# Performance work log

Hardware: AMD Instinct MI355X
Metric: run time of the kernel (lower is better)

Reference implementation:

```python
import jax, jax.numpy as jnp
import numpy as np

OUT_IMG = 256
OUT_MSK = 64


def _src_coords(n_out, size):
    # F.interpolate bilinear align_corners=False source coordinates, clamped to edge
    sizef = size.astype(jnp.float32)
    t = (jnp.arange(n_out, dtype=jnp.float32) + 0.5) * (sizef / n_out) - 0.5
    t = jnp.clip(t, 0.0, sizef - 1.0)
    t0 = jnp.floor(t).astype(jnp.int32)
    t1 = jnp.minimum(t0 + 1, size - 1)
    return t0, t1, t - t0.astype(jnp.float32)


def _per_sample(x_img, x_msk, x_bg, pad, sel, color):
    # x_img [3,H,W] float, x_msk [H,W] bool, x_bg [3,Hb,Wb], pad [4] int (l,r,t,b)
    H, W = x_msk.shape
    ys = jnp.any(x_msk, axis=1)
    xs = jnp.any(x_msk, axis=0)
    iy = jnp.arange(H)
    ix = jnp.arange(W)
    miny = jnp.min(jnp.where(ys, iy, H))
    maxy = jnp.max(jnp.where(ys, iy, -1))
    minx = jnp.min(jnp.where(xs, ix, W))
    maxx = jnp.max(jnp.where(xs, ix, -1))
    h = maxy - miny + 1
    w = maxx - minx + 1
    left, right, top, bot = pad[0], pad[1], pad[2], pad[3]
    Hp = h + top + bot   # padded crop height
    Wp = w + left + right  # padded crop width
    # background: real bg image or solid random color (c[ii][-1] > 2 branch)
    bg_sel = jnp.where(sel > 2, x_bg, jnp.broadcast_to(color[:, None, None], x_bg.shape))

    def mask_at(P, Q):
        # value of the padded-cropped mask at integer padded coords (P, Q)
        in_crop = (P >= top) & (P < top + h) & (Q >= left) & (Q < left + w)
        r = jnp.clip(miny + P - top, 0, H - 1)
        c = jnp.clip(minx + Q - left, 0, W - 1)
        return in_crop & x_msk[r, c], r, c

    def sample_img(py, px):
        # composited padded image at integer coords (py x px grid) -> [3,Ho,Wo]
        P = py[:, None]
        Q = px[None, :]
        m, r, c = mask_at(P, Q)
        iv = x_img[:, r, c]
        bv = bg_sel[:, P, Q]
        return jnp.where(m[None], iv, bv)

    def sample_msk(py, px):
        m, _, _ = mask_at(py[:, None], px[None, :])
        return m.astype(jnp.float32)

    def bilinear(sample_fn, n_out, ch_leading):
        y0, y1, wy = _src_coords(n_out, Hp)
        x0, x1, wx = _src_coords(n_out, Wp)
        s00 = sample_fn(y0, x0)
        s01 = sample_fn(y0, x1)
        s10 = sample_fn(y1, x0)
        s11 = sample_fn(y1, x1)
        wy_ = wy[:, None]
        wx_ = wx[None, :]
        if ch_leading:
            wy_ = wy_[None]
            wx_ = wx_[None]
        top_row = s00 * (1.0 - wx_) + s01 * wx_
        bot_row = s10 * (1.0 - wx_) + s11 * wx_
        return top_row * (1.0 - wy_) + bot_row * wy_

    img_out = bilinear(sample_img, OUT_IMG, True)        # [3,256,256]
    msk_out = bilinear(sample_msk, OUT_MSK, False)[None]  # [1,64,64]
    return img_out, msk_out


def _rgb_to_hsv(x):
    r, g, b = x[:, 0], x[:, 1], x[:, 2]
    mx = jnp.max(x, axis=1)
    mn = jnp.min(x, axis=1)
    d = mx - mn
    ds = jnp.where(d > 0, d, 1.0)
    hr = ((g - b) / ds) % 6.0
    hg = (b - r) / ds + 2.0
    hb = (r - g) / ds + 4.0
    hch = jnp.where(mx == r, hr, jnp.where(mx == g, hg, hb)) / 6.0
    hch = jnp.where(d > 0, hch, 0.0)
    s = jnp.where(mx > 0, d / jnp.where(mx > 0, mx, 1.0), 0.0)
    return hch, s, mx


def _hsv_to_rgb(hch, s, v):
    h6 = hch * 6.0
    i = jnp.floor(h6)
    f = h6 - i
    p = v * (1.0 - s)
    q = v * (1.0 - f * s)
    t = v * (1.0 - (1.0 - f) * s)
    im = i.astype(jnp.int32) % 6
    conds = [im == 0, im == 1, im == 2, im == 3, im == 4, im == 5]
    r = jnp.select(conds, [v, q, p, p, t, v])
    g = jnp.select(conds, [t, v, v, q, p, p])
    b = jnp.select(conds, [p, p, t, v, v, q])
    return jnp.stack([r, g, b], axis=1)


def _color_jitter(img, jit):
    # ColorJitter(0.1, 0.1, 0.1, 0.1) with explicit per-sample factors
    b = (0.9 + 0.2 * jit[:, 0])[:, None, None, None]
    c = (0.9 + 0.2 * jit[:, 1])[:, None, None, None]
    s = (0.9 + 0.2 * jit[:, 2])[:, None, None, None]
    hd = (-0.1 + 0.2 * jit[:, 3])[:, None, None]
    img = jnp.clip(img * b, 0.0, 1.0)
    gray = (0.299 * img[:, 0] + 0.587 * img[:, 1] + 0.114 * img[:, 2])[:, None]
    mean = jnp.mean(gray, axis=(2, 3), keepdims=True)
    img = jnp.clip(c * img + (1.0 - c) * mean, 0.0, 1.0)
    gray = (0.299 * img[:, 0] + 0.587 * img[:, 1] + 0.114 * img[:, 2])[:, None]
    img = jnp.clip(s * img + (1.0 - s) * gray, 0.0, 1.0)
    hch, sa, v = _rgb_to_hsv(img)
    hch = (hch + hd) % 1.0
    return jnp.clip(_hsv_to_rgb(hch, sa, v), 0.0, 1.0)


def setup_inputs() -> dict:
    key = jax.random.key(0)
    ks = jax.random.split(key, 7)
    B, H, W = 64, 448, 448
    return {
        "img": jax.random.uniform(ks[0], (B, 3, H, W), jnp.float32),
        "ms": jax.random.uniform(ks[1], (B, 1, H, W), jnp.float32),
        "bg": jax.random.uniform(ks[2], (B, 3, H + 40, W + 40), jnp.float32),
        "pads": jax.random.randint(ks[3], (B, 4), 0, 20, jnp.int32),
        "csel": jax.random.randint(ks[4], (B,), 0, 20, jnp.int32),
        "rand_color": jax.random.uniform(ks[5], (B, 3), jnp.float32),
        "jitter": jax.random.uniform(ks[6], (B, 4), jnp.float32),
    }


def reference(img, ms, bg, pads, csel, rand_color, jitter):
    mask = ms[:, 0] > 0.5
    img_out, msk_out = jax.vmap(_per_sample)(img, mask, bg, pads, csel, rand_color)
    img_out = _color_jitter(img_out, jitter)
    return img_out, msk_out
```

## Files before the change

kernel.cpp:

```cpp
#include <hip/hip_runtime.h>

#define H_IN 448
#define W_IN 448
#define HW_IN (H_IN * W_IN)
#define BGW 488
#define BGHW (BGW * BGW)
#define OUTI 256
#define OUTI_PIX (OUTI * OUTI)
#define OUTM 64
#define B_SAMPLES 64
#define BBOX_CHUNKS 16
#define BBOX_ROWS (H_IN / BBOX_CHUNKS)
#define BITS_STRIDE 8

typedef unsigned long long u64;

__device__ __forceinline__ float clamp01(float x) { return fminf(fmaxf(x, 0.f), 1.f); }
__device__ __forceinline__ int clampi(int x, int lo, int hi) { return min(max(x, lo), hi); }

__device__ __forceinline__ void gld_lds16(const float4* g, float4* l) {
    __builtin_amdgcn_global_load_lds(
        (const __attribute__((address_space(1))) void*)g,
        (__attribute__((address_space(3))) void*)l, 16, 0, 0);
}

__global__ void k_bbox(const float* __restrict__ ms, int* __restrict__ bbox,
                       u64* __restrict__ bits) {
    int b = blockIdx.y, chunk = blockIdx.x;
    int tid = threadIdx.x;
    int wave = tid >> 6, lane = tid & 63;
    const float* msB = ms + (size_t)b * HW_IN;
    u64* bitsB = bits + (size_t)b * H_IN * BITS_STRIDE;

    int miny = H_IN, maxy = -1, minx = W_IN, maxx = -1;
    for (int rr = wave; rr < BBOX_ROWS; rr += 4) {
        int row = chunk * BBOX_ROWS + rr;
        const float4* rowp = (const float4*)(msB + (size_t)row * W_IN);
#pragma unroll
        for (int sub = 0; sub < 2; ++sub) {
            int c4 = sub * 64 + lane;
            bool valid = c4 < (W_IN / 4);
            float4 v = rowp[min(c4, W_IN / 4 - 1)];
            bool a0 = valid && (v.x > 0.5f);
            bool a1 = valid && (v.y > 0.5f);
            bool a2 = valid && (v.z > 0.5f);
            bool a3 = valid && (v.w > 0.5f);
            u64 b0 = __ballot(a0), b1 = __ballot(a1), b2 = __ballot(a2), b3 = __ballot(a3);
            if (a0 | a1 | a2 | a3) {
                miny = min(miny, row); maxy = max(maxy, row);
                int xb = c4 * 4;
                if (a0) { minx = min(minx, xb);     maxx = max(maxx, xb); }
                if (a1) { minx = min(minx, xb + 1); maxx = max(maxx, xb + 1); }
                if (a2) { minx = min(minx, xb + 2); maxx = max(maxx, xb + 2); }
                if (a3) { minx = min(minx, xb + 3); maxx = max(maxx, xb + 3); }
            }
            if (lane < 4) {
                u64 w = (lane == 0) ? b0 : (lane == 1) ? b1 : (lane == 2) ? b2 : b3;
                bitsB[(size_t)row * BITS_STRIDE + sub * 4 + lane] = w;
            }
        }
    }
    __shared__ int s[4];
    if (tid == 0) { s[0] = H_IN; s[1] = -1; s[2] = W_IN; s[3] = -1; }
    __syncthreads();
    atomicMin(&s[0], miny); atomicMax(&s[1], maxy);
    atomicMin(&s[2], minx); atomicMax(&s[3], maxx);
    __syncthreads();
    if (tid == 0) {
        atomicMin(&bbox[b * 4 + 0], s[0]);
        atomicMin(&bbox[b * 4 + 1], -s[1]);
        atomicMin(&bbox[b * 4 + 2], s[2]);
        atomicMin(&bbox[b * 4 + 3], -s[3]);
    }
}

struct Geo {
    int miny, minx, h, w, top, left, Hp, Wp;
};
__device__ __forceinline__ Geo load_geo(const int* __restrict__ bbox,
                                        const int* __restrict__ pads, int b) {
    Geo g;
    g.miny = bbox[b * 4 + 0];
    int maxy = -bbox[b * 4 + 1];
    g.minx = bbox[b * 4 + 2];
    int maxx = -bbox[b * 4 + 3];
    int left = pads[b * 4 + 0], right = pads[b * 4 + 1];
    int top = pads[b * 4 + 2], bot = pads[b * 4 + 3];
    g.h = maxy - g.miny + 1;
    g.w = maxx - g.minx + 1;
    g.top = top; g.left = left;
    g.Hp = g.h + top + bot;
    g.Wp = g.w + left + right;
    return g;
}

__device__ __forceinline__ void src_coord(int i, int n_out, int size,
                                          int& t0, int& t1, float& frac) {
    float sizef = (float)size;
    float t = (i + 0.5f) * (sizef / (float)n_out) - 0.5f;
    t = fminf(fmaxf(t, 0.f), sizef - 1.f);
    t0 = (int)floorf(t);
    t1 = min(t0 + 1, size - 1);
    frac = t - (float)t0;
}

__device__ __forceinline__ bool mask_bit(const u64* rowbits, int c) {
    u64 w = rowbits[((c >> 8) << 2) | (c & 3)];
    return (w >> ((c >> 2) & 63)) & 1ULL;
}

__global__ void __launch_bounds__(256) k_resize_img(
        const float* __restrict__ img, const float* __restrict__ bg,
        const int* __restrict__ pads, const int* __restrict__ csel,
        const float* __restrict__ rcol, const float* __restrict__ jit,
        const int* __restrict__ bbox, const u64* __restrict__ bits,
        float* __restrict__ out, float* __restrict__ partials) {
    int oy = blockIdx.x;
    int b = blockIdx.y;
    int tid = threadIdx.x;
    int wave = tid >> 6, lane = tid & 63;

    Geo g = load_geo(bbox, pads, b);
    bool useBg = csel[b] > 2;
    float c0 = rcol[b * 3 + 0], c1 = rcol[b * 3 + 1], c2 = rcol[b * 3 + 2];
    float bfac = 0.9f + 0.2f * jit[b * 4 + 0];

    int y0, y1; float wy;
    src_coord(oy, OUTI, g.Hp, y0, y1, wy);
    int r0 = clampi(g.miny + y0 - g.top, 0, H_IN - 1);
    int r1 = clampi(g.miny + y1 - g.top, 0, H_IN - 1);
    bool incy0 = (y0 >= g.top) && (y0 < g.top + g.h);
    bool incy1 = (y1 >= g.top) && (y1 < g.top + g.h);

    __shared__ float s_im[6][W_IN];
    __shared__ float s_bg[6][BGW];
    __shared__ u64 s_bits[2][BITS_STRIDE];
    __shared__ float ls[4];

    const float* imB = img + (size_t)b * 3 * HW_IN;
    const u64* bitsB = bits + (size_t)b * H_IN * BITS_STRIDE;

#pragma unroll
    for (int k = 0; k < 3; ++k) {
        int item = wave + k * 4;
        int p = item >> 1;
        int ck = item & 1;
        int row = (p >= 3) ? r1 : r0;
        int ch = (p >= 3) ? (p - 3) : p;
        const float4* src =
            (const float4*)(imB + (size_t)ch * HW_IN + (size_t)row * W_IN) + ck * 64 + lane;
        float4* dst = (float4*)(&s_im[p][0]) + ck * 64;
        if (lane < (ck ? 48 : 64)) gld_lds16(src, dst);
    }
    if (useBg) {
        const float* bgB = bg + (size_t)b * 3 * BGHW;
#pragma unroll
        for (int k = 0; k < 3; ++k) {
            int item = wave + k * 4;
            int p = item >> 1;
            int ck = item & 1;
            int row = (p >= 3) ? y1 : y0;
            int ch = (p >= 3) ? (p - 3) : p;
            const float4* src =
                (const float4*)(bgB + (size_t)ch * BGHW + (size_t)row * BGW) + ck * 64 + lane;
            float4* dst = (float4*)(&s_bg[p][0]) + ck * 64;
            if (lane < (ck ? 58 : 64)) gld_lds16(src, dst);
        }
    }
    if (tid < 16) {
        int ky = tid >> 3, idx = tid & 7;
        s_bits[ky][idx] = bitsB[(size_t)(ky ? r1 : r0) * BITS_STRIDE + idx];
    }
    __syncthreads();

    int x0, x1; float wx;
    src_coord(tid, OUTI, g.Wp, x0, x1, wx);

    float acc0 = 0.f, acc1 = 0.f, acc2 = 0.f;
#pragma unroll
    for (int tap = 0; tap < 4; ++tap) {
        int ky = tap >> 1;
        int ky3 = ky * 3;
        int Q = (tap & 1) ? x1 : x0;
        float wgt = (ky ? wy : 1.f - wy) * ((tap & 1) ? wx : 1.f - wx);
        bool incy = ky ? incy1 : incy0;
        bool in_crop = incy && (Q >= g.left) && (Q < g.left + g.w);
        int c = clampi(g.minx + Q - g.left, 0, W_IN - 1);
        bool mm = in_crop && mask_bit(s_bits[ky], c);
        float i0 = s_im[ky3 + 0][c], i1 = s_im[ky3 + 1][c], i2 = s_im[ky3 + 2][c];
        float b0, b1, b2;
        if (useBg) {
            b0 = s_bg[ky3 + 0][Q]; b1 = s_bg[ky3 + 1][Q]; b2 = s_bg[ky3 + 2][Q];
        } else {
            b0 = c0; b1 = c1; b2 = c2;
        }
        acc0 += wgt * (mm ? i0 : b0);
        acc1 += wgt * (mm ? i1 : b1);
        acc2 += wgt * (mm ? i2 : b2);
    }
    float o0 = clamp01(acc0 * bfac);
    float o1 = clamp01(acc1 * bfac);
    float o2 = clamp01(acc2 * bfac);
    size_t o = (size_t)b * 3 * OUTI_PIX + (size_t)oy * OUTI + tid;
    out[o] = o0;
    out[o + OUTI_PIX] = o1;
    out[o + 2 * OUTI_PIX] = o2;

    float gsum = 0.299f * o0 + 0.587f * o1 + 0.114f * o2;
#pragma unroll
    for (int off = 32; off > 0; off >>= 1) gsum += __shfl_down(gsum, off, 64);
    int wid = tid >> 6, lane2 = tid & 63;
    if (lane2 == 0) ls[wid] = gsum;
    __syncthreads();
    if (tid == 0)
        partials[b * 256 + oy] = ls[0] + ls[1] + ls[2] + ls[3];
}

__global__ void k_resize_msk(const u64* __restrict__ bits, const int* __restrict__ pads,
                             const int* __restrict__ bbox, float* __restrict__ outm) {
    int b = blockIdx.y;
    int pix = blockIdx.x * blockDim.x + threadIdx.x;
    int oy = pix >> 6, ox = pix & 63;

    Geo g = load_geo(bbox, pads, b);
    int y0, y1, x0, x1; float wy, wx;
    src_coord(oy, OUTM, g.Hp, y0, y1, wy);
    src_coord(ox, OUTM, g.Wp, x0, x1, wx);

    const u64* bitsB = bits + (size_t)b * H_IN * BITS_STRIDE;
    float acc = 0.f;
#pragma unroll
    for (int tap = 0; tap < 4; ++tap) {
        int P = (tap & 2) ? y1 : y0;
        int Q = (tap & 1) ? x1 : x0;
        float wgt = ((tap & 2) ? wy : 1.f - wy) * ((tap & 1) ? wx : 1.f - wx);
        bool in_crop = (P >= g.top) && (P < g.top + g.h) && (Q >= g.left) && (Q < g.left + g.w);
        int r = clampi(g.miny + P - g.top, 0, H_IN - 1);
        int c = clampi(g.minx + Q - g.left, 0, W_IN - 1);
        bool mm = in_crop && mask_bit(bitsB + (size_t)r * BITS_STRIDE, c);
        acc += wgt * (mm ? 1.f : 0.f);
    }
    outm[(size_t)b * (OUTM * OUTM) + pix] = acc;
}

__device__ __forceinline__ void jitter_px(float& r, float& g, float& bl,
                                          float cc, float ssf, float hd, float mean) {
    r = clamp01(cc * r + (1.f - cc) * mean);
    g = clamp01(cc * g + (1.f - cc) * mean);
    bl = clamp01(cc * bl + (1.f - cc) * mean);
    float gray = 0.299f * r + 0.587f * g + 0.114f * bl;
    r = clamp01(ssf * r + (1.f - ssf) * gray);
    g = clamp01(ssf * g + (1.f - ssf) * gray);
    bl = clamp01(ssf * bl + (1.f - ssf) * gray);
    float mx = fmaxf(r, fmaxf(g, bl));
    float mn = fminf(r, fminf(g, bl));
    float d = mx - mn;
    float dsv = (d > 0.f) ? d : 1.f;
    float hch;
    if (mx == r) {
        float t = (g - bl) / dsv;
        t = fmodf(t, 6.f);
        if (t < 0.f) t += 6.f;
        hch = t;
    } else if (mx == g) {
        hch = (bl - r) / dsv + 2.f;
    } else {
        hch = (r - g) / dsv + 4.f;
    }
    hch = (d > 0.f) ? hch * (1.f / 6.f) : 0.f;
    float sat = (mx > 0.f) ? d / mx : 0.f;
    float v = mx;
    float hh = hch + hd;
    hh -= floorf(hh);
    float h6 = hh * 6.f;
    float fi = floorf(h6);
    float f = h6 - fi;
    float pp = v * (1.f - sat);
    float q = v * (1.f - f * sat);
    float t = v * (1.f - (1.f - f) * sat);
    int im = ((int)fi) % 6;
    float ro, go, bo;
    switch (im) {
        case 0: ro = v;  go = t;  bo = pp; break;
        case 1: ro = q;  go = v;  bo = pp; break;
        case 2: ro = pp; go = v;  bo = t;  break;
        case 3: ro = pp; go = q;  bo = v;  break;
        case 4: ro = t;  go = pp; bo = v;  break;
        default: ro = v; go = pp; bo = q;  break;
    }
    r = clamp01(ro); g = clamp01(go); bl = clamp01(bo);
}

__global__ void k_jitter(float* __restrict__ io, const float* __restrict__ jit,
                         const float* __restrict__ partials) {
    int b = blockIdx.y;
    int tid = threadIdx.x;

    float pv = partials[b * 256 + tid];
#pragma unroll
    for (int off = 32; off > 0; off >>= 1) pv += __shfl_down(pv, off, 64);
    __shared__ float ls[4];
    int wid = tid >> 6, lane = tid & 63;
    if (lane == 0) ls[wid] = pv;
    __syncthreads();
    float mean = (ls[0] + ls[1] + ls[2] + ls[3]) * (1.f / (float)OUTI_PIX);

    float cc = 0.9f + 0.2f * jit[b * 4 + 1];
    float ssf = 0.9f + 0.2f * jit[b * 4 + 2];
    float hd = -0.1f + 0.2f * jit[b * 4 + 3];

    int idx4 = blockIdx.x * blockDim.x + tid;
    float4* pr = (float4*)(io + (size_t)b * 3 * OUTI_PIX) + idx4;
    float4* pg = pr + OUTI_PIX / 4;
    float4* pb = pr + 2 * (OUTI_PIX / 4);
    float4 r = *pr, g = *pg, bl = *pb;

    jitter_px(r.x, g.x, bl.x, cc, ssf, hd, mean);
    jitter_px(r.y, g.y, bl.y, cc, ssf, hd, mean);
    jitter_px(r.z, g.z, bl.z, cc, ssf, hd, mean);
    jitter_px(r.w, g.w, bl.w, cc, ssf, hd, mean);

    *pr = r; *pg = g; *pb = bl;
}

extern "C" void kernel_launch(void* const* d_in, const int* in_sizes, int n_in,
                              void* d_out, int out_size, void* d_ws, size_t ws_size,
                              hipStream_t stream) {
    const float* img = (const float*)d_in[0];
    const float* ms = (const float*)d_in[1];
    const float* bg = (const float*)d_in[2];
    const int* pads = (const int*)d_in[3];
    const int* csel = (const int*)d_in[4];
    const float* rcol = (const float*)d_in[5];
    const float* jit = (const float*)d_in[6];
    float* out = (float*)d_out;

    int* bbox = (int*)d_ws;
    float* partials = (float*)((char*)d_ws + 1024);
    u64* bits = (u64*)((char*)d_ws + 1024 + B_SAMPLES * 256 * sizeof(float));
    float* outm = out + (size_t)B_SAMPLES * 3 * OUTI_PIX;

    hipMemsetAsync(bbox, 0x7F, B_SAMPLES * 4 * sizeof(int), stream);

    k_bbox<<<dim3(BBOX_CHUNKS, B_SAMPLES), 256, 0, stream>>>(ms, bbox, bits);
    k_resize_img<<<dim3(OUTI, B_SAMPLES), 256, 0, stream>>>(
        img, bg, pads, csel, rcol, jit, bbox, bits, out, partials);
    k_resize_msk<<<dim3((OUTM * OUTM) / 256, B_SAMPLES), 256, 0, stream>>>(
        bits, pads, bbox, outm);
    k_jitter<<<dim3(OUTI_PIX / 4 / 256, B_SAMPLES), 256, 0, stream>>>(out, jit, partials);
}
```

Baseline: 122.4 us.

## Process eight output rows per block with double-buffered async LDS staging

The image resize kernel now has each block handle eight consecutive output rows instead of one. It double-buffers the source image, background and mask-bit rows in LDS, prefetching the next row via global_load_lds while computing the current one, with hand-tuned vmcnt waits. The horizontal taps are also restructured to read adjacent LDS entries and lerp, and partial sums per block shrink to one per group. This trades launch and per-block setup overhead and load latency exposure for fewer blocks (less parallelism), doubled LDS use, and fragile manual waitcnt accounting.

```diff
diff --git a/kernel.cpp b/kernel.cpp
--- a/kernel.cpp
+++ b/kernel.cpp
@@ -12,8 +12,12 @@
 #define BBOX_CHUNKS 16
 #define BBOX_ROWS (H_IN / BBOX_CHUNKS)
 #define BITS_STRIDE 8
+#define RPB 8
+#define NGRP (OUTI / RPB)
 
 typedef unsigned long long u64;
+
+#define WAITV(N) asm volatile("s_waitcnt vmcnt(" #N ")" ::: "memory")
 
 __device__ __forceinline__ float clamp01(float x) { return fminf(fmaxf(x, 0.f), 1.f); }
 __device__ __forceinline__ int clampi(int x, int lo, int hi) { return min(max(x, lo), hi); }
@@ -104,9 +108,60 @@
     frac = t - (float)t0;
 }
 
-__device__ __forceinline__ bool mask_bit(const u64* rowbits, int c) {
+__device__ __forceinline__ bool bit_at(const u64* rowbits, int c) {
     u64 w = rowbits[((c >> 8) << 2) | (c & 3)];
     return (w >> ((c >> 2) & 63)) & 1ULL;
+}
+
+struct RowGeom {
+    int y0, y1, r0, r1;
+    float wy;
+    bool incy0, incy1;
+};
+__device__ __forceinline__ RowGeom row_geom(const Geo& g, int oy) {
+    RowGeom rg;
+    src_coord(oy, OUTI, g.Hp, rg.y0, rg.y1, rg.wy);
+    rg.r0 = clampi(g.miny + rg.y0 - g.top, 0, H_IN - 1);
+    rg.r1 = clampi(g.miny + rg.y1 - g.top, 0, H_IN - 1);
+    rg.incy0 = (rg.y0 >= g.top) && (rg.y0 < g.top + g.h);
+    rg.incy1 = (rg.y1 >= g.top) && (rg.y1 < g.top + g.h);
+    return rg;
+}
+
+__device__ __forceinline__ void stage_async(
+        const float* imB, const float* bgB, const u64* bitsB, bool useBg,
+        const RowGeom& rg, int wave, int lane,
+        float (*im)[W_IN], float (*bgp)[BGW], u64 (*bt)[BITS_STRIDE]) {
+#pragma unroll
+    for (int k = 0; k < 3; ++k) {
+        int chunk = wave * 3 + k;
+        int p = chunk >> 1, ck = chunk & 1;
+        int row = (p >= 3) ? rg.r1 : rg.r0;
+        int ch = (p >= 3) ? p - 3 : p;
+        const float4* src =
+            (const float4*)(imB + (size_t)ch * HW_IN + (size_t)row * W_IN) + ck * 64 + lane;
+        float4* dst = (float4*)(&im[p][0]) + ck * 64;
+        if (lane < (ck ? 48 : 64)) gld_lds16(src, dst);
+    }
+    if (useBg) {
+#pragma unroll
+        for (int k = 0; k < 3; ++k) {
+            int chunk = wave * 3 + k;
+            int p = chunk >> 1, ck = chunk & 1;
+            int row = (p >= 3) ? rg.y1 : rg.y0;
+            int ch = (p >= 3) ? p - 3 : p;
+            const float4* src =
+                (const float4*)(bgB + (size_t)ch * BGHW + (size_t)row * BGW) + ck * 64 + lane;
+            float4* dst = (float4*)(&bgp[p][0]) + ck * 64;
+            if (lane < (ck ? 58 : 64)) gld_lds16(src, dst);
+        }
+    }
+    if (wave < 2) {
+        int row = wave ? rg.r1 : rg.r0;
+        const float4* src = (const float4*)(bitsB + (size_t)row * BITS_STRIDE) + lane;
+        float4* dst = (float4*)(&bt[wave][0]);
+        if (lane < 4) gld_lds16(src, dst);
+    }
 }
 
 __global__ void __launch_bounds__(256) k_resize_img(
@@ -115,7 +170,7 @@
         const float* __restrict__ rcol, const float* __restrict__ jit,
         const int* __restrict__ bbox, const u64* __restrict__ bits,
         float* __restrict__ out, float* __restrict__ partials) {
-    int oy = blockIdx.x;
+    int grp = blockIdx.x;
     int b = blockIdx.y;
     int tid = threadIdx.x;
     int wave = tid >> 6, lane = tid & 63;
@@ -125,95 +180,94 @@
     float c0 = rcol[b * 3 + 0], c1 = rcol[b * 3 + 1], c2 = rcol[b * 3 + 2];
     float bfac = 0.9f + 0.2f * jit[b * 4 + 0];
 
-    int y0, y1; float wy;
-    src_coord(oy, OUTI, g.Hp, y0, y1, wy);
-    int r0 = clampi(g.miny + y0 - g.top, 0, H_IN - 1);
-    int r1 = clampi(g.miny + y1 - g.top, 0, H_IN - 1);
-    bool incy0 = (y0 >= g.top) && (y0 < g.top + g.h);
-    bool incy1 = (y1 >= g.top) && (y1 < g.top + g.h);
-
-    __shared__ float s_im[6][W_IN];
-    __shared__ float s_bg[6][BGW];
-    __shared__ u64 s_bits[2][BITS_STRIDE];
-    __shared__ float ls[4];
-
-    const float* imB = img + (size_t)b * 3 * HW_IN;
-    const u64* bitsB = bits + (size_t)b * H_IN * BITS_STRIDE;
-
-#pragma unroll
-    for (int k = 0; k < 3; ++k) {
-        int item = wave + k * 4;
-        int p = item >> 1;
-        int ck = item & 1;
-        int row = (p >= 3) ? r1 : r0;
-        int ch = (p >= 3) ? (p - 3) : p;
-        const float4* src =
-            (const float4*)(imB + (size_t)ch * HW_IN + (size_t)row * W_IN) + ck * 64 + lane;
-        float4* dst = (float4*)(&s_im[p][0]) + ck * 64;
-        if (lane < (ck ? 48 : 64)) gld_lds16(src, dst);
-    }
-    if (useBg) {
-        const float* bgB = bg + (size_t)b * 3 * BGHW;
-#pragma unroll
-        for (int k = 0; k < 3; ++k) {
-            int item = wave + k * 4;
-            int p = item >> 1;
-            int ck = item & 1;
-            int row = (p >= 3) ? y1 : y0;
-            int ch = (p >= 3) ? (p - 3) : p;
-            const float4* src =
-                (const float4*)(bgB + (size_t)ch * BGHW + (size_t)row * BGW) + ck * 64 + lane;
-            float4* dst = (float4*)(&s_bg[p][0]) + ck * 64;
-            if (lane < (ck ? 58 : 64)) gld_lds16(src, dst);
-        }
-    }
-    if (tid < 16) {
-        int ky = tid >> 3, idx = tid & 7;
-        s_bits[ky][idx] = bitsB[(size_t)(ky ? r1 : r0) * BITS_STRIDE + idx];
-    }
-    __syncthreads();
-
     int x0, x1; float wx;
     src_coord(tid, OUTI, g.Wp, x0, x1, wx);
-
-    float acc0 = 0.f, acc1 = 0.f, acc2 = 0.f;
-#pragma unroll
-    for (int tap = 0; tap < 4; ++tap) {
-        int ky = tap >> 1;
-        int ky3 = ky * 3;
-        int Q = (tap & 1) ? x1 : x0;
-        float wgt = (ky ? wy : 1.f - wy) * ((tap & 1) ? wx : 1.f - wx);
-        bool incy = ky ? incy1 : incy0;
-        bool in_crop = incy && (Q >= g.left) && (Q < g.left + g.w);
-        int c = clampi(g.minx + Q - g.left, 0, W_IN - 1);
-        bool mm = in_crop && mask_bit(s_bits[ky], c);
-        float i0 = s_im[ky3 + 0][c], i1 = s_im[ky3 + 1][c], i2 = s_im[ky3 + 2][c];
-        float b0, b1, b2;
-        if (useBg) {
-            b0 = s_bg[ky3 + 0][Q]; b1 = s_bg[ky3 + 1][Q]; b2 = s_bg[ky3 + 2][Q];
+    int cA = clampi(g.minx + x0 - g.left, 0, W_IN - 1);
+    int cB = clampi(g.minx + x1 - g.left, 0, W_IN - 1);
+    bool inxA = (x0 >= g.left) && (x0 < g.left + g.w);
+    bool inxB = (x1 >= g.left) && (x1 < g.left + g.w);
+
+    __shared__ __align__(16) float s_im[2][6][W_IN];
+    __shared__ __align__(16) float s_bg[2][6][BGW];
+    __shared__ __align__(16) u64 s_bits[2][2][BITS_STRIDE];
+    __shared__ float ls[4];
+
+    const float* imB = img + (size_t)b * 3 * HW_IN;
+    const float* bgB = bg + (size_t)b * 3 * BGHW;
+    const u64* bitsB = bits + (size_t)b * H_IN * BITS_STRIDE;
+
+    stage_async(imB, bgB, bitsB, useBg, row_geom(g, grp * RPB), wave, lane,
+                s_im[0], s_bg[0], s_bits[0]);
+
+    float gacc = 0.f;
+#pragma unroll
+    for (int t = 0; t < RPB; ++t) {
+        const int d = t & 1;
+        if (t + 1 < RPB) {
+            stage_async(imB, bgB, bitsB, useBg, row_geom(g, grp * RPB + t + 1),
+                        wave, lane, s_im[d ^ 1], s_bg[d ^ 1], s_bits[d ^ 1]);
+        }
+        if (t + 1 < RPB) {
+            if (useBg) { if (wave < 2) WAITV(7); else WAITV(6); }
+            else       { if (wave < 2) WAITV(4); else WAITV(3); }
         } else {
-            b0 = c0; b1 = c1; b2 = c2;
+            WAITV(0);
         }
-        acc0 += wgt * (mm ? i0 : b0);
-        acc1 += wgt * (mm ? i1 : b1);
-        acc2 += wgt * (mm ? i2 : b2);
-    }
-    float o0 = clamp01(acc0 * bfac);
-    float o1 = clamp01(acc1 * bfac);
-    float o2 = clamp01(acc2 * bfac);
-    size_t o = (size_t)b * 3 * OUTI_PIX + (size_t)oy * OUTI + tid;
-    out[o] = o0;
-    out[o + OUTI_PIX] = o1;
-    out[o + 2 * OUTI_PIX] = o2;
-
-    float gsum = 0.299f * o0 + 0.587f * o1 + 0.114f * o2;
-#pragma unroll
-    for (int off = 32; off > 0; off >>= 1) gsum += __shfl_down(gsum, off, 64);
-    int wid = tid >> 6, lane2 = tid & 63;
-    if (lane2 == 0) ls[wid] = gsum;
+        __builtin_amdgcn_sched_barrier(0);
+        __builtin_amdgcn_s_barrier();
+        __builtin_amdgcn_sched_barrier(0);
+
+        RowGeom rg = row_geom(g, grp * RPB + t);
+        float acc0 = 0.f, acc1 = 0.f, acc2 = 0.f;
+#pragma unroll
+        for (int ky = 0; ky < 2; ++ky) {
+            bool incy = ky ? rg.incy1 : rg.incy0;
+            bool mmA = incy && inxA && bit_at(s_bits[d][ky], cA);
+            bool mmB = incy && inxB && bit_at(s_bits[d][ky], cB);
+            float wyk = ky ? rg.wy : 1.f - rg.wy;
+            int ky3 = ky * 3;
+#pragma unroll
+            for (int ch = 0; ch < 3; ++ch) {
+                float iA = s_im[d][ky3 + ch][cA];
+                float iAp = s_im[d][ky3 + ch][cA + 1];
+                float iB = (cB > cA) ? iAp : iA;
+                float bA, bB;
+                if (useBg) {
+                    float bgA = s_bg[d][ky3 + ch][x0];
+                    float bgAp = s_bg[d][ky3 + ch][x0 + 1];
+                    bA = bgA;
+                    bB = (x1 > x0) ? bgAp : bgA;
+                } else {
+                    bA = bB = (ch == 0) ? c0 : (ch == 1) ? c1 : c2;
+                }
+                float vA = mmA ? iA : bA;
+                float vB = mmB ? iB : bB;
+                float hv = vA + wx * (vB - vA);
+                if (ch == 0) acc0 += wyk * hv;
+                else if (ch == 1) acc1 += wyk * hv;
+                else acc2 += wyk * hv;
+            }
+        }
+        float o0 = clamp01(acc0 * bfac);
+        float o1 = clamp01(acc1 * bfac);
+        float o2 = clamp01(acc2 * bfac);
+        size_t o = (size_t)b * 3 * OUTI_PIX + (size_t)(grp * RPB + t) * OUTI + tid;
+        out[o] = o0;
+        out[o + OUTI_PIX] = o1;
+        out[o + 2 * OUTI_PIX] = o2;
+        gacc += 0.299f * o0 + 0.587f * o1 + 0.114f * o2;
+
+        __builtin_amdgcn_sched_barrier(0);
+        __builtin_amdgcn_s_barrier();
+    }
+
+#pragma unroll
+    for (int off = 32; off > 0; off >>= 1) gacc += __shfl_down(gacc, off, 64);
+    __syncthreads();
+    if (lane == 0) ls[wave] = gacc;
     __syncthreads();
     if (tid == 0)
-        partials[b * 256 + oy] = ls[0] + ls[1] + ls[2] + ls[3];
+        partials[b * NGRP + grp] = ls[0] + ls[1] + ls[2] + ls[3];
 }
 
 __global__ void k_resize_msk(const u64* __restrict__ bits, const int* __restrict__ pads,
@@ -237,7 +291,7 @@
         bool in_crop = (P >= g.top) && (P < g.top + g.h) && (Q >= g.left) && (Q < g.left + g.w);
         int r = clampi(g.miny + P - g.top, 0, H_IN - 1);
         int c = clampi(g.minx + Q - g.left, 0, W_IN - 1);
-        bool mm = in_crop && mask_bit(bitsB + (size_t)r * BITS_STRIDE, c);
+        bool mm = in_crop && bit_at(bitsB + (size_t)r * BITS_STRIDE, c);
         acc += wgt * (mm ? 1.f : 0.f);
     }
     outm[(size_t)b * (OUTM * OUTM) + pix] = acc;
@@ -296,7 +350,7 @@
     int b = blockIdx.y;
     int tid = threadIdx.x;
 
-    float pv = partials[b * 256 + tid];
+    float pv = (tid < NGRP) ? partials[b * NGRP + tid] : 0.f;
 #pragma unroll
     for (int off = 32; off > 0; off >>= 1) pv += __shfl_down(pv, off, 64);
     __shared__ float ls[4];
@@ -337,13 +391,13 @@
 
     int* bbox = (int*)d_ws;
     float* partials = (float*)((char*)d_ws + 1024);
-    u64* bits = (u64*)((char*)d_ws + 1024 + B_SAMPLES * 256 * sizeof(float));
+    u64* bits = (u64*)((char*)d_ws + 1024 + 65536);
     float* outm = out + (size_t)B_SAMPLES * 3 * OUTI_PIX;
 
     hipMemsetAsync(bbox, 0x7F, B_SAMPLES * 4 * sizeof(int), stream);
 
     k_bbox<<<dim3(BBOX_CHUNKS, B_SAMPLES), 256, 0, stream>>>(ms, bbox, bits);
-    k_resize_img<<<dim3(OUTI, B_SAMPLES), 256, 0, stream>>>(
+    k_resize_img<<<dim3(NGRP, B_SAMPLES), 256, 0, stream>>>(
         img, bg, pads, csel, rcol, jit, bbox, bits, out, partials);
     k_resize_msk<<<dim3((OUTM * OUTM) / 256, B_SAMPLES), 256, 0, stream>>>(
         bits, pads, bbox, outm);
```

Result: slower. 127.0 us (+3.7%).
